# Kernel optimization log

Hardware: AMD Instinct MI355X
Metric: run time of the kernel (lower is better)

Reference implementation:

```python
import jax, jax.numpy as jnp
import numpy as np

EPS = 1e-5
N_HEADS = 8

def _layernorm(h, g, b):
    mu = jnp.mean(h, axis=-1, keepdims=True)
    var = jnp.mean((h - mu) ** 2, axis=-1, keepdims=True)
    return g * (h - mu) * jax.lax.rsqrt(var + EPS) + b

def _mlp_ln(x, W1, b1, W2, b2, g, beta):
    # Linear -> SiLU -> Linear -> LayerNorm (torch nn.Sequential processor)
    h = jax.nn.silu(x @ W1.T + b1)
    h = h @ W2.T + b2
    return _layernorm(h, g, beta)

def setup_inputs() -> dict:
    key = jax.random.key(0)
    ks = jax.random.split(key, 16)
    B, S, D = 4, 2048, 1024
    M, P, C = 128, 256, 512
    def lin(k, o, i):
        return (jax.random.normal(k, (o, i), jnp.float32) / np.sqrt(i)).astype(jnp.float32)
    inp = {}
    inp['x'] = jax.random.normal(ks[0], (B, S, D), jnp.float32)
    inp['scale_types'] = jax.random.randint(ks[1], (B, S), 0, 3)
    for name, dim, k1, k2 in [('mol', M, 2, 3), ('path', P, 4, 5), ('cell', C, 6, 7)]:
        inp[name + '_W1'] = lin(ks[k1], dim, D)
        inp[name + '_b1'] = jnp.zeros((dim,), jnp.float32)
        inp[name + '_W2'] = lin(ks[k2], dim, dim)
        inp[name + '_b2'] = jnp.zeros((dim,), jnp.float32)
        inp[name + '_g'] = jnp.ones((dim,), jnp.float32)
        inp[name + '_beta'] = jnp.zeros((dim,), jnp.float32)
    inp['int_W1'] = lin(ks[8], D, M + P + C)
    inp['int_b1'] = jnp.zeros((D,), jnp.float32)
    inp['int_W2'] = lin(ks[9], D, D)
    inp['int_b2'] = jnp.zeros((D,), jnp.float32)
    inp['int_g'] = jnp.ones((D,), jnp.float32)
    inp['int_beta'] = jnp.zeros((D,), jnp.float32)
    inp['attn_Wqkv'] = lin(ks[10], 3 * D, D)
    inp['attn_bqkv'] = jnp.zeros((3 * D,), jnp.float32)
    inp['attn_Wo'] = lin(ks[11], D, D)
    inp['attn_bo'] = jnp.zeros((D,), jnp.float32)
    inp['scale_w'] = jnp.ones((3,), jnp.float32) / 3.0
    return inp

def reference(x, scale_types,
              mol_W1, mol_b1, mol_W2, mol_b2, mol_g, mol_beta,
              path_W1, path_b1, path_W2, path_b2, path_g, path_beta,
              cell_W1, cell_b1, cell_W2, cell_b2, cell_g, cell_beta,
              int_W1, int_b1, int_W2, int_b2, int_g, int_beta,
              attn_Wqkv, attn_bqkv, attn_Wo, attn_bo, scale_w):
    B, S, D = x.shape
    # per-token routing: each token goes through exactly one expert; the
    # other two scale outputs are zeros (mask instead of Python loop).
    mol = _mlp_ln(x, mol_W1, mol_b1, mol_W2, mol_b2, mol_g, mol_beta) * (scale_types == 0)[..., None]
    path = _mlp_ln(x, path_W1, path_b1, path_W2, path_b2, path_g, path_beta) * (scale_types == 1)[..., None]
    cell = _mlp_ln(x, cell_W1, cell_b1, cell_W2, cell_b2, cell_g, cell_beta) * (scale_types == 2)[..., None]
    cat = jnp.concatenate([mol, path, cell], axis=-1)  # [B,S,M+P+C]
    integrated = _layernorm(jax.nn.silu(cat @ int_W1.T + int_b1) @ int_W2.T + int_b2, int_g, int_beta)
    # torch nn.MultiheadAttention (batch_first, self-attention)
    Dh = D // N_HEADS
    qkv = integrated @ attn_Wqkv.T + attn_bqkv  # [B,S,3D]
    q, k, v = jnp.split(qkv, 3, axis=-1)
    q = q.reshape(B, S, N_HEADS, Dh)
    k = k.reshape(B, S, N_HEADS, Dh)
    v = v.reshape(B, S, N_HEADS, Dh)
    scores = jnp.einsum('bqhd,bkhd->bhqk', q, k) / np.sqrt(Dh).astype(np.float32)
    attn = jax.nn.softmax(scores, axis=-1)
    o = jnp.einsum('bhqk,bkhd->bqhd', attn, v).reshape(B, S, D)
    attended = o @ attn_Wo.T + attn_bo
    w = jax.nn.softmax(scale_w, axis=0)
    final = integrated + w[0] * attended
    return (final, mol, path, cell)
```

## Files before the change

### kernel.cpp

```cpp
#include <hip/hip_runtime.h>
#include <cstdint>
#include <cstddef>

typedef unsigned short u16;
typedef unsigned int u32;
typedef short bf16x8 __attribute__((ext_vector_type(8)));
typedef float f32x4 __attribute__((ext_vector_type(4)));

__device__ __forceinline__ float bf2f(u16 u){
  union { u32 i; float f; } c; c.i = ((u32)u) << 16; return c.f;
}
__device__ __forceinline__ u16 f2bf(float f){
  union { float f; u32 i; } c; c.f = f;
  u32 r = c.i + 0x7FFFu + ((c.i >> 16) & 1u);
  return (u16)(r >> 16);
}
__device__ __forceinline__ void gload_lds16(const void* g, void* l){
  __builtin_amdgcn_global_load_lds(
      (const __attribute__((address_space(1))) u32*)g,
      (__attribute__((address_space(3))) u32*)l, 16, 0, 0);
}

struct ConvArgs {
  const float* src[11];
  u16* dst[11];
  u32 base[12];
};
__global__ __launch_bounds__(256)
void f32_to_bf16_multi(ConvArgs a){
  u32 i = blockIdx.x * 256 + threadIdx.x;
  if (i >= a.base[11]) return;
  int j = 0;
  #pragma unroll
  for (int k = 1; k < 11; ++k) j += (i >= a.base[k]);
  u32 li = i - a.base[j];
  const float4* s = (const float4*)a.src[j] + (size_t)li * 2;
  float4 va = s[0], vb = s[1];
  u16 o[8] = {f2bf(va.x),f2bf(va.y),f2bf(va.z),f2bf(va.w),
              f2bf(vb.x),f2bf(vb.y),f2bf(vb.z),f2bf(vb.w)};
  *(uint4*)(a.dst[j] + (size_t)li * 8) = *(const uint4*)o;
}

__global__ __launch_bounds__(256)
void concat3_f32(const float* __restrict__ a, const float* __restrict__ b,
                 const float* __restrict__ c, float* __restrict__ d){
  int i = blockIdx.x * 256 + threadIdx.x;
  if (i < 128) d[i] = a[i];
  else if (i < 384) d[i] = b[i - 128];
  else if (i < 896) d[i] = c[i - 384];
}

template<int EPI>
__device__ __forceinline__ void gemm_body(
    const u16* __restrict__ A, const u16* __restrict__ W,
    const float* __restrict__ bias, void* __restrict__ Cv,
    int N, int K, int lda, int ldc,
    const u16* __restrict__ I, const float* __restrict__ sw,
    int bx, int by)
{
  __shared__ __align__(16) u16 As[128*64];
  __shared__ __align__(16) u16 Bs[128*64];
  const int tid  = threadIdx.x;
  const int lane = tid & 63;
  const int wave = tid >> 6;
  const int wr = wave >> 1, wc = wave & 1;
  const int m0 = by * 128, n0 = bx * 128;

  f32x4 acc[4][4];
  #pragma unroll
  for (int r=0;r<4;++r)
    #pragma unroll
    for (int c=0;c<4;++c)
      #pragma unroll
      for (int e=0;e<4;++e) acc[r][c][e] = 0.f;

  int srow[4], soff[4];
  #pragma unroll
  for (int j=0;j<4;++j){
    int rr = (wave*4 + j)*8 + (lane>>3);
    srow[j] = rr;
    soff[j] = ((lane & 7) ^ (rr & 7)) * 8;
  }

  for (int k0 = 0; k0 < K; k0 += 64){
    #pragma unroll
    for (int j=0;j<4;++j){
      gload_lds16(A + (size_t)(m0 + srow[j])*lda + k0 + soff[j], As + (wave*4+j)*512);
      gload_lds16(W + (size_t)(n0 + srow[j])*K   + k0 + soff[j], Bs + (wave*4+j)*512);
    }
    __syncthreads();
    #pragma unroll
    for (int ks=0; ks<2; ++ks){
      bf16x8 af[4], bfr[4];
      #pragma unroll
      for (int r=0;r<4;++r){
        int row = wr*64 + r*16 + (lane&15);
        int cs  = (ks*4 + (lane>>4)) ^ (row & 7);
        af[r] = *(const bf16x8*)(As + row*64 + cs*8);
      }
      #pragma unroll
      for (int c=0;c<4;++c){
        int row = wc*64 + c*16 + (lane&15);
        int cs  = (ks*4 + (lane>>4)) ^ (row & 7);
        bfr[c] = *(const bf16x8*)(Bs + row*64 + cs*8);
      }
      #pragma unroll
      for (int r=0;r<4;++r)
        #pragma unroll
        for (int c=0;c<4;++c)
          acc[r][c] = __builtin_amdgcn_mfma_f32_16x16x32_bf16(af[r], bfr[c], acc[r][c], 0,0,0);
    }
    __syncthreads();
  }

  float w0 = 0.f;
  if (EPI == 2){
    float s0 = sw[0], s1 = sw[1], s2 = sw[2];
    float mx = fmaxf(s0, fmaxf(s1, s2));
    float e0 = __expf(s0-mx), e1 = __expf(s1-mx), e2 = __expf(s2-mx);
    w0 = e0 / (e0 + e1 + e2);
  }
  u16*   C16 = (u16*)Cv;
  float* C32 = (float*)Cv;
  #pragma unroll
  for (int c=0;c<4;++c){
    int col = n0 + wc*64 + c*16 + (lane&15);
    float bv = bias[col];
    #pragma unroll
    for (int r=0;r<4;++r){
      int rbase = m0 + wr*64 + r*16 + (lane>>4)*4;
      #pragma unroll
      for (int e=0;e<4;++e){
        int row = rbase + e;
        float v = acc[r][c][e] + bv;
        if (EPI == 1) v = v / (1.f + __expf(-v));
        if (EPI == 2){
          v = bf2f(I[(size_t)row*ldc + col]) + w0 * v;
          C32[(size_t)row*ldc + col] = v;
        } else {
          C16[(size_t)row*ldc + col] = f2bf(v);
        }
      }
    }
  }
}

template<int EPI>
__global__ __launch_bounds__(256, 2)
void gemm_bt(const u16* __restrict__ A, const u16* __restrict__ W,
             const float* __restrict__ bias, void* __restrict__ Cv,
             int N, int K, int lda, int ldc,
             const u16* __restrict__ I, const float* __restrict__ sw)
{
  gemm_body<EPI>(A, W, bias, Cv, N, K, lda, ldc, I, sw, blockIdx.x, blockIdx.y);
}

__global__ __launch_bounds__(256, 2)
void gemm_w2group(const u16* __restrict__ S1, u16* __restrict__ S2,
                  const u16* __restrict__ w0, const u16* __restrict__ w1,
                  const u16* __restrict__ w2, const float* __restrict__ b0,
                  const float* __restrict__ b1, const float* __restrict__ b2)
{
  int bx = blockIdx.x;
  if (bx < 64){
    gemm_body<0>(S1, w0, b0, S2, 128, 128, 896, 896, nullptr, nullptr, 0, bx);
  } else if (bx < 192){
    int l = bx - 64;
    gemm_body<0>(S1+128, w1, b1, S2+128, 256, 256, 896, 896, nullptr, nullptr, l>>6, l&63);
  } else {
    int l = bx - 192;
    gemm_body<0>(S1+384, w2, b2, S2+384, 512, 512, 896, 896, nullptr, nullptr, l>>6, l&63);
  }
}

template<int D>
__device__ __forceinline__ void ln_body_masked(
    u16* __restrict__ H, int ldh, const float* __restrict__ g,
    const float* __restrict__ beta, const int* __restrict__ st,
    int eid, float* __restrict__ outp)
{
  const int tid = threadIdx.x, lane = tid & 63, wave = tid >> 6;
  const int token = blockIdx.x * 4 + wave;
  constexpr int VPT = D / 64;
  float v[VPT];
  u16* row = H + (size_t)token * ldh + lane * VPT;
  #pragma unroll
  for (int i=0;i<VPT/2;++i){
    u32 u = ((const u32*)row)[i];
    v[2*i]   = bf2f((u16)(u & 0xFFFFu));
    v[2*i+1] = bf2f((u16)(u >> 16));
  }
  float s = 0.f;
  #pragma unroll
  for (int i=0;i<VPT;++i) s += v[i];
  #pragma unroll
  for (int off=1; off<64; off<<=1) s += __shfl_xor(s, off);
  float mu = s * (1.f / D);
  float q = 0.f;
  #pragma unroll
  for (int i=0;i<VPT;++i){ float d = v[i] - mu; q += d * d; }
  #pragma unroll
  for (int off=1; off<64; off<<=1) q += __shfl_xor(q, off);
  float rs = rsqrtf(q * (1.f / D) + 1e-5f);
  float msk = (st[token] == eid) ? 1.f : 0.f;
  #pragma unroll
  for (int i=0;i<VPT;++i){
    float gg = g[lane*VPT + i];
    float bb = beta[lane*VPT + i];
    float val = (gg * (v[i] - mu) * rs + bb) * msk;
    outp[(size_t)token * D + lane * VPT + i] = val;
    row[i] = f2bf(val);
  }
}

__global__ __launch_bounds__(256, 4)
void ln_expert(u16* __restrict__ S2,
               const float* __restrict__ g0, const float* __restrict__ be0,
               const float* __restrict__ g1, const float* __restrict__ be1,
               const float* __restrict__ g2, const float* __restrict__ be2,
               const int* __restrict__ st,
               float* __restrict__ o0, float* __restrict__ o1,
               float* __restrict__ o2)
{
  if (blockIdx.y == 0)      ln_body_masked<128>(S2,     896, g0, be0, st, 0, o0);
  else if (blockIdx.y == 1) ln_body_masked<256>(S2+128, 896, g1, be1, st, 1, o1);
  else                      ln_body_masked<512>(S2+384, 896, g2, be2, st, 2, o2);
}

__global__ __launch_bounds__(256, 4)
void ln_int(const u16* __restrict__ H, const float* __restrict__ g,
            const float* __restrict__ beta, u16* __restrict__ outp)
{
  const int tid = threadIdx.x, lane = tid & 63, wave = tid >> 6;
  const int token = blockIdx.x * 4 + wave;
  constexpr int D = 1024, VPT = 16;
  float v[VPT];
  const u16* row = H + (size_t)token * D + lane * VPT;
  #pragma unroll
  for (int i=0;i<VPT/2;++i){
    u32 u = ((const u32*)row)[i];
    v[2*i]   = bf2f((u16)(u & 0xFFFFu));
    v[2*i+1] = bf2f((u16)(u >> 16));
  }
  float s = 0.f;
  #pragma unroll
  for (int i=0;i<VPT;++i) s += v[i];
  #pragma unroll
  for (int off=1; off<64; off<<=1) s += __shfl_xor(s, off);
  float mu = s * (1.f / D);
  float q = 0.f;
  #pragma unroll
  for (int i=0;i<VPT;++i){ float d = v[i] - mu; q += d * d; }
  #pragma unroll
  for (int off=1; off<64; off<<=1) q += __shfl_xor(q, off);
  float rs = rsqrtf(q * (1.f / D) + 1e-5f);
  #pragma unroll
  for (int i=0;i<VPT;++i){
    float val = g[lane*VPT + i] * (v[i] - mu) * rs + beta[lane*VPT + i];
    outp[(size_t)token * D + lane * VPT + i] = f2bf(val);
  }
}

__global__ __launch_bounds__(256)
void transpose_v(const u16* __restrict__ qkv, u16* __restrict__ vt)
{
  __shared__ __align__(16) u16 T[64*72];
  const int tid = threadIdx.x;
  const int tt = blockIdx.x;
  const int dt = blockIdx.y;
  const int bh = blockIdx.z;
  const int b = bh >> 3, h = bh & 7;
  #pragma unroll
  for (int i=0;i<2;++i){
    int idx = tid + 256*i;
    int r = idx >> 3, c8 = idx & 7;
    const uint4* src = (const uint4*)(qkv + (size_t)(b*2048 + tt*64 + r)*3072
                                      + 2048 + h*128 + dt*64 + c8*8);
    *(uint4*)(T + r*72 + ((c8 ^ (r>>3)) & 7)*8) = *src;
  }
  __syncthreads();
  #pragma unroll
  for (int i=0;i<2;++i){
    int idx = tid + 256*i;
    int dr = idx >> 3, tc = idx & 7;
    u16 tmp[8];
    #pragma unroll
    for (int j=0;j<8;++j){
      int kap = tc*8 + j;
      int hp = kap >> 5, r2 = kap & 31;
      int srow = hp*32 + ((r2 & 1) ? 16 + (r2 >> 1) : (r2 >> 1));
      tmp[j] = T[srow*72 + (((dr>>3) ^ (srow>>3)) & 7)*8 + (dr & 7)];
    }
    *(uint4*)(vt + ((size_t)bh*128 + dt*64 + dr)*2048 + tt*64 + tc*8) = *(const uint4*)tmp;
  }
}

__global__ __launch_bounds__(256, 4)
void flash_attn(const u16* __restrict__ qkv, const u16* __restrict__ vt,
                u16* __restrict__ o)
{
  __shared__ __align__(16) u16 Ks[8192];
  __shared__ __align__(16) u16 Vs[8192];
  __shared__ __align__(16) u16 Ps[4*1024];
  const int tid = threadIdx.x, lane = tid & 63, wave = tid >> 6;
  const int b = blockIdx.z, h = blockIdx.y, q0 = blockIdx.x * 64;
  const float cl2   = 0.12751791892f;
  const float DEFER = 90.50966799187809f;

  bf16x8 qreg[4];
  {
    const u16* qrow = qkv + (size_t)(b*2048 + q0 + wave*16 + (lane&15))*3072
                      + h*128 + (lane>>4)*8;
    #pragma unroll
    for (int kk=0;kk<4;++kk) qreg[kk] = *(const bf16x8*)(qrow + kk*32);
  }
  asm volatile("s_waitcnt vmcnt(0)" ::: "memory");

  const u16* ksrc[4]; const u16* vsrc[4]; int cdst[4];
  #pragma unroll
  for (int i=0;i<4;++i){
    int cidx = (wave*4 + i)*64 + lane;
    int krow = cidx >> 4, kcs = cidx & 15;
    int kcsrc = (kcs & 8) | ((kcs & 7) ^ (krow & 7));
    ksrc[i] = qkv + (size_t)(b*2048 + krow)*3072 + h*128 + 1024 + kcsrc*8;
    int vd = cidx >> 3, vcs = cidx & 7;
    vsrc[i] = vt + ((size_t)(b*8 + h)*128 + vd)*2048 + (vcs ^ (vd & 7))*8;
    cdst[i] = cidx * 8;
  }

  int koff[16];
  #pragma unroll
  for (int kk=0;kk<4;++kk)
    #pragma unroll
    for (int cb=0;cb<4;++cb){
      int row  = (lane&15) + 16*cb;
      int c    = kk*4 + (lane>>4);
      int slot = (c & 8) | ((c & 7) ^ (row & 7));
      koff[kk*4+cb] = (row*128 + slot*8) * 2;
    }
  int voff[16];
  #pragma unroll
  for (int kk=0;kk<2;++kk)
    #pragma unroll
    for (int f=0;f<8;++f){
      int d = f*16 + (lane&15);
      int c = kk*4 + (lane>>4);
      voff[kk*8+f] = (d*64 + (c ^ (d & 7))*8) * 2;
    }
  int pwoff[8];
  #pragma unroll
  for (int e=0;e<4;++e){
    int prow = (lane>>4)*4 + e;
    int j01 = lane & 15;
    int j23 = 16 + (lane & 15);
    pwoff[e*2]   = (prow*32 + (((((j01>>2) ^ (prow&7)) & 7)<<2) | (j01&3))) * 4;
    pwoff[e*2+1] = (prow*32 + (((((j23>>2) ^ (prow&7)) & 7)<<2) | (j23&3))) * 4;
  }
  int proff[2];
  #pragma unroll
  for (int kk=0;kk<2;++kk){
    int prow = lane & 15;
    int pc   = kk*4 + (lane>>4);
    proff[kk] = (prow*64 + ((pc ^ (prow & 7)) & 7)*8) * 2;
  }

  auto stageK = [&](int kt){
    #pragma unroll
    for (int i=0;i<4;++i) gload_lds16(ksrc[i] + (size_t)kt*196608, Ks + cdst[i]);
  };
  auto stageV = [&](int kt){
    #pragma unroll
    for (int i=0;i<4;++i) gload_lds16(vsrc[i] + kt*64, Vs + cdst[i]);
  };

  f32x4 oacc[8];
  #pragma unroll
  for (int f=0;f<8;++f)
    #pragma unroll
    for (int e=0;e<4;++e) oacc[f][e] = 0.f;
  float m_run[4] = {-3e38f,-3e38f,-3e38f,-3e38f};
  float l_run[4] = {0.f,0.f,0.f,0.f};
  const char* KsB = (const char*)Ks;
  const char* VsB = (const char*)Vs;
  char* PsWB = (char*)(Ps + wave*1024);

  stageK(0);
  stageV(0);
  asm volatile("s_waitcnt vmcnt(4)" ::: "memory");
  __builtin_amdgcn_s_barrier();
  __builtin_amdgcn_sched_barrier(0);

  for (int kt=0; kt<32; ++kt){
    f32x4 s[4];
    #pragma unroll
    for (int cb=0;cb<4;++cb)
      #pragma unroll
      for (int e=0;e<4;++e) s[cb][e] = 0.f;
    __builtin_amdgcn_s_setprio(1);
    #pragma unroll
    for (int kk=0;kk<4;++kk){
      #pragma unroll
      for (int cb=0;cb<4;++cb){
        bf16x8 bk = *(const bf16x8*)(KsB + koff[kk*4+cb]);
        s[cb] = __builtin_amdgcn_mfma_f32_16x16x32_bf16(qreg[kk], bk, s[cb], 0,0,0);
      }
    }
    __builtin_amdgcn_s_setprio(0);
    asm volatile("s_waitcnt lgkmcnt(0)" ::: "memory");
    __builtin_amdgcn_sched_barrier(0);
    __builtin_amdgcn_s_barrier();
    __builtin_amdgcn_sched_barrier(0);
    stageK((kt+1)&31);

    #pragma unroll
    for (int e=0;e<4;++e){
      float t0 = s[0][e], t1 = s[1][e], t2 = s[2][e], t3 = s[3][e];
      float lmx = fmaxf(fmaxf(t0,t1), fmaxf(t2,t3));
      if (__any(lmx > m_run[e] + DEFER)){
        float mx = lmx;
        #pragma unroll
        for (int off=1; off<16; off<<=1) mx = fmaxf(mx, __shfl_xor(mx, off));
        float mnew = fmaxf(m_run[e], mx);
        float a = exp2f((m_run[e] - mnew) * cl2);
        m_run[e] = mnew;
        l_run[e] *= a;
        #pragma unroll
        for (int f=0;f<8;++f) oacc[f][e] *= a;
      }
      float ms = m_run[e];
      float p0 = exp2f((t0 - ms)*cl2), p1 = exp2f((t1 - ms)*cl2);
      float p2 = exp2f((t2 - ms)*cl2), p3 = exp2f((t3 - ms)*cl2);
      l_run[e] += (p0 + p1) + (p2 + p3);
      u32 c01, c23;
      asm("v_cvt_pk_bf16_f32 %0, %1, %2" : "=v"(c01) : "v"(p0), "v"(p1));
      asm("v_cvt_pk_bf16_f32 %0, %1, %2" : "=v"(c23) : "v"(p2), "v"(p3));
      *(u32*)(PsWB + pwoff[e*2])   = c01;
      *(u32*)(PsWB + pwoff[e*2+1]) = c23;
    }

    asm volatile("s_waitcnt vmcnt(4)" ::: "memory");
    __builtin_amdgcn_sched_barrier(0);
    __builtin_amdgcn_s_barrier();
    __builtin_amdgcn_sched_barrier(0);

    __builtin_amdgcn_s_setprio(1);
    #pragma unroll
    for (int kk=0;kk<2;++kk){
      bf16x8 pa = *(const bf16x8*)(PsWB + proff[kk]);
      #pragma unroll
      for (int f=0;f<8;++f){
        bf16x8 vb = *(const bf16x8*)(VsB + voff[kk*8+f]);
        oacc[f] = __builtin_amdgcn_mfma_f32_16x16x32_bf16(pa, vb, oacc[f], 0,0,0);
      }
    }
    __builtin_amdgcn_s_setprio(0);
    asm volatile("s_waitcnt lgkmcnt(0) vmcnt(0)" ::: "memory");
    __builtin_amdgcn_sched_barrier(0);
    __builtin_amdgcn_s_barrier();
    __builtin_amdgcn_sched_barrier(0);
    if (kt + 1 < 32) stageV(kt+1);
  }

  #pragma unroll
  for (int e=0;e<4;++e){
    float l = l_run[e];
    #pragma unroll
    for (int off=1; off<16; off<<=1) l += __shfl_xor(l, off);
    l_run[e] = 1.f / l;
  }
  #pragma unroll
  for (int f=0;f<8;++f)
    #pragma unroll
    for (int e=0;e<4;++e){
      int row = q0 + wave*16 + (lane>>4)*4 + e;
      int col = h*128 + f*16 + (lane&15);
      o[(size_t)(b*2048 + row)*1024 + col] = f2bf(oacc[f][e] * l_run[e]);
    }
}

extern "C" void kernel_launch(void* const* d_in, const int* in_sizes, int n_in,
                              void* d_out, int out_size, void* d_ws, size_t ws_size,
                              hipStream_t stream)
{
  const float* x         = (const float*)d_in[0];
  const int*   stypes    = (const int*)d_in[1];
  const float* mol_W1    = (const float*)d_in[2];
  const float* mol_b1    = (const float*)d_in[3];
  const float* mol_W2    = (const float*)d_in[4];
  const float* mol_b2    = (const float*)d_in[5];
  const float* mol_g     = (const float*)d_in[6];
  const float* mol_beta  = (const float*)d_in[7];
  const float* path_W1   = (const float*)d_in[8];
  const float* path_b1   = (const float*)d_in[9];
  const float* path_W2   = (const float*)d_in[10];
  const float* path_b2   = (const float*)d_in[11];
  const float* path_g    = (const float*)d_in[12];
  const float* path_beta = (const float*)d_in[13];
  const float* cell_W1   = (const float*)d_in[14];
  const float* cell_b1   = (const float*)d_in[15];
  const float* cell_W2   = (const float*)d_in[16];
  const float* cell_b2   = (const float*)d_in[17];
  const float* cell_g    = (const float*)d_in[18];
  const float* cell_beta = (const float*)d_in[19];
  const float* int_W1    = (const float*)d_in[20];
  const float* int_b1    = (const float*)d_in[21];
  const float* int_W2    = (const float*)d_in[22];
  const float* int_b2    = (const float*)d_in[23];
  const float* int_g     = (const float*)d_in[24];
  const float* int_beta  = (const float*)d_in[25];
  const float* attn_Wqkv = (const float*)d_in[26];
  const float* attn_bqkv = (const float*)d_in[27];
  const float* attn_Wo   = (const float*)d_in[28];
  const float* attn_bo   = (const float*)d_in[29];
  const float* scale_w   = (const float*)d_in[30];

  float* out_final = (float*)d_out;
  float* out_mol   = out_final + 8388608;
  float* out_path  = out_mol   + 1048576;
  float* out_cell  = out_path  + 2097152;

  u16* ws    = (u16*)d_ws;
  u16* qkv   = ws;
  u16* integ = qkv   + 25165824;
  u16* S1    = integ + 8388608;
  u16* S2    = S1    + 8388608;
  u16* wb    = S2    + 8388608;
  u16* xb    = qkv;

  u16* w1f    = wb;
  u16* molW2b = w1f    + 917504;
  u16* pathW2b= molW2b + 16384;
  u16* cellW2b= pathW2b+ 65536;
  u16* intW1b = cellW2b+ 262144;
  u16* intW2b = intW1b + 917504;
  u16* qkvWb  = intW2b + 1048576;
  u16* woWb   = qkvWb  + 3145728;
  float* fbias= (float*)(woWb + 1048576);

  dim3 blk(256);

  ConvArgs ca;
  const float* srcs[11] = {x, mol_W1, path_W1, cell_W1, mol_W2, path_W2,
                           cell_W2, int_W1, int_W2, attn_Wqkv, attn_Wo};
  u16* dsts[11] = {xb, w1f, w1f + 131072, w1f + 393216, molW2b, pathW2b,
                   cellW2b, intW1b, intW2b, qkvWb, woWb};
  u32 n8s[11] = {1048576, 16384, 32768, 65536, 2048, 8192,
                 32768, 114688, 131072, 393216, 131072};
  u32 acc8 = 0;
  for (int i=0;i<11;++i){ ca.src[i]=srcs[i]; ca.dst[i]=dsts[i]; ca.base[i]=acc8; acc8+=n8s[i]; }
  ca.base[11] = acc8;
  f32_to_bf16_multi<<<(acc8 + 255)/256, blk, 0, stream>>>(ca);
  concat3_f32<<<4, blk, 0, stream>>>(mol_b1, path_b1, cell_b1, fbias);

  gemm_bt<1><<<dim3(7,64), blk, 0, stream>>>(xb, w1f, fbias, S1, 896, 1024, 1024, 896, nullptr, nullptr);
  gemm_w2group<<<448, blk, 0, stream>>>(S1, S2, molW2b, pathW2b, cellW2b,
                                        mol_b2, path_b2, cell_b2);
  ln_expert<<<dim3(2048,3), blk, 0, stream>>>(S2, mol_g, mol_beta, path_g,
                                              path_beta, cell_g, cell_beta,
                                              stypes, out_mol, out_path, out_cell);

  gemm_bt<1><<<dim3(8,64), blk, 0, stream>>>(S2, intW1b, int_b1, S1, 1024, 896,  896,  1024, nullptr, nullptr);
  gemm_bt<0><<<dim3(8,64), blk, 0, stream>>>(S1, intW2b, int_b2, S2, 1024, 1024, 1024, 1024, nullptr, nullptr);
  ln_int<<<2048, blk, 0, stream>>>(S2, int_g, int_beta, integ);

  gemm_bt<0><<<dim3(24,64), blk, 0, stream>>>(integ, qkvWb, attn_bqkv, qkv, 3072, 1024, 1024, 3072, nullptr, nullptr);
  transpose_v<<<dim3(32,2,32), blk, 0, stream>>>(qkv, S2);
  flash_attn<<<dim3(32,8,4), blk, 0, stream>>>(qkv, S2, S1);

  gemm_bt<2><<<dim3(8,64), blk, 0, stream>>>(S1, woWb, attn_bo, out_final, 1024, 1024, 1024, 1024, integ, scale_w);
}
```

Measured before the change: 332.2 us.

## Fuse V transpose into QKV GEMM via swapped-operand V^T tile epilogue

The QKV projection now runs as one launch. The Q/K blocks use the normal GEMM. The V part is computed directly as Wv·integ^T, with an epilogue that writes the permuted transposed layout flash attention expects. This removes the separate transpose_v kernel and its extra read and write of V. The cost is a scattered 2-byte store pattern in the new epilogue. Separately, flash attention's K/V staging now advances pointers incrementally instead of recomputing offsets. After the last iteration the K prefetch no longer wraps to tile 0 and reads past the current batch's K range.

```diff
diff --git a/kernel.cpp b/kernel.cpp
--- a/kernel.cpp
+++ b/kernel.cpp
@@ -125,18 +125,29 @@
   #pragma unroll
   for (int c=0;c<4;++c){
     int col = n0 + wc*64 + c*16 + (lane&15);
-    float bv = bias[col];
+    float bv = 0.f;
+    size_t vtb = 0;
+    if (EPI == 3){
+      int tl = (col & 2047) >> 6, pos = col & 63;
+      int p2 = pos & 31, hp = pos >> 5;
+      int kap = hp*32 + (p2 < 16 ? 2*p2 : 2*(p2-16)+1);
+      vtb = (size_t)(col >> 11) * 2097152 + (size_t)(tl*64 + kap);
+    } else {
+      bv = bias[col];
+    }
     #pragma unroll
     for (int r=0;r<4;++r){
       int rbase = m0 + wr*64 + r*16 + (lane>>4)*4;
       #pragma unroll
       for (int e=0;e<4;++e){
         int row = rbase + e;
-        float v = acc[r][c][e] + bv;
+        float v = acc[r][c][e] + (EPI==3 ? bias[row] : bv);
         if (EPI == 1) v = v / (1.f + __expf(-v));
         if (EPI == 2){
           v = bf2f(I[(size_t)row*ldc + col]) + w0 * v;
           C32[(size_t)row*ldc + col] = v;
+        } else if (EPI == 3){
+          C16[vtb + (size_t)row*2048] = f2bf(v);
         } else {
           C16[(size_t)row*ldc + col] = f2bf(v);
         }
@@ -173,6 +184,22 @@
   }
 }
 
+__global__ __launch_bounds__(256, 2)
+void gemm_qkv_vt(const u16* __restrict__ integ, const u16* __restrict__ Wqkv,
+                 const float* __restrict__ bqkv, u16* __restrict__ qkv,
+                 u16* __restrict__ vt)
+{
+  int bx = blockIdx.x;
+  if (bx < 1024){
+    gemm_body<0>(integ, Wqkv, bqkv, qkv, 2048, 1024, 1024, 3072,
+                 nullptr, nullptr, bx & 15, bx >> 4);
+  } else {
+    int l = bx - 1024;
+    gemm_body<3>(Wqkv + (size_t)2048*1024, integ, bqkv + 2048, vt, 8192, 1024,
+                 1024, 2048, nullptr, nullptr, l & 63, l >> 6);
+  }
+}
+
 template<int D>
 __device__ __forceinline__ void ln_body_masked(
     u16* __restrict__ H, int ldh, const float* __restrict__ g,
@@ -261,40 +288,6 @@
   }
 }
 
-__global__ __launch_bounds__(256)
-void transpose_v(const u16* __restrict__ qkv, u16* __restrict__ vt)
-{
-  __shared__ __align__(16) u16 T[64*72];
-  const int tid = threadIdx.x;
-  const int tt = blockIdx.x;
-  const int dt = blockIdx.y;
-  const int bh = blockIdx.z;
-  const int b = bh >> 3, h = bh & 7;
-  #pragma unroll
-  for (int i=0;i<2;++i){
-    int idx = tid + 256*i;
-    int r = idx >> 3, c8 = idx & 7;
-    const uint4* src = (const uint4*)(qkv + (size_t)(b*2048 + tt*64 + r)*3072
-                                      + 2048 + h*128 + dt*64 + c8*8);
-    *(uint4*)(T + r*72 + ((c8 ^ (r>>3)) & 7)*8) = *src;
-  }
-  __syncthreads();
-  #pragma unroll
-  for (int i=0;i<2;++i){
-    int idx = tid + 256*i;
-    int dr = idx >> 3, tc = idx & 7;
-    u16 tmp[8];
-    #pragma unroll
-    for (int j=0;j<8;++j){
-      int kap = tc*8 + j;
-      int hp = kap >> 5, r2 = kap & 31;
-      int srow = hp*32 + ((r2 & 1) ? 16 + (r2 >> 1) : (r2 >> 1));
-      tmp[j] = T[srow*72 + (((dr>>3) ^ (srow>>3)) & 7)*8 + (dr & 7)];
-    }
-    *(uint4*)(vt + ((size_t)bh*128 + dt*64 + dr)*2048 + tt*64 + tc*8) = *(const uint4*)tmp;
-  }
-}
-
 __global__ __launch_bounds__(256, 4)
 void flash_attn(const u16* __restrict__ qkv, const u16* __restrict__ vt,
                 u16* __restrict__ o)
@@ -364,13 +357,13 @@
     proff[kk] = (prow*64 + ((pc ^ (prow & 7)) & 7)*8) * 2;
   }
 
-  auto stageK = [&](int kt){
-    #pragma unroll
-    for (int i=0;i<4;++i) gload_lds16(ksrc[i] + (size_t)kt*196608, Ks + cdst[i]);
+  auto stageK = [&](){
+    #pragma unroll
+    for (int i=0;i<4;++i){ gload_lds16(ksrc[i], Ks + cdst[i]); ksrc[i] += 196608; }
   };
-  auto stageV = [&](int kt){
-    #pragma unroll
-    for (int i=0;i<4;++i) gload_lds16(vsrc[i] + kt*64, Vs + cdst[i]);
+  auto stageV = [&](){
+    #pragma unroll
+    for (int i=0;i<4;++i){ gload_lds16(vsrc[i], Vs + cdst[i]); vsrc[i] += 64; }
   };
 
   f32x4 oacc[8];
@@ -384,8 +377,8 @@
   const char* VsB = (const char*)Vs;
   char* PsWB = (char*)(Ps + wave*1024);
 
-  stageK(0);
-  stageV(0);
+  stageK();
+  stageV();
   asm volatile("s_waitcnt vmcnt(4)" ::: "memory");
   __builtin_amdgcn_s_barrier();
   __builtin_amdgcn_sched_barrier(0);
@@ -410,7 +403,7 @@
     __builtin_amdgcn_sched_barrier(0);
     __builtin_amdgcn_s_barrier();
     __builtin_amdgcn_sched_barrier(0);
-    stageK((kt+1)&31);
+    stageK();
 
     #pragma unroll
     for (int e=0;e<4;++e){
@@ -458,7 +451,7 @@
     __builtin_amdgcn_sched_barrier(0);
     __builtin_amdgcn_s_barrier();
     __builtin_amdgcn_sched_barrier(0);
-    if (kt + 1 < 32) stageV(kt+1);
+    if (kt + 1 < 32) stageV();
   }
 
   #pragma unroll
@@ -563,8 +556,7 @@
   gemm_bt<0><<<dim3(8,64), blk, 0, stream>>>(S1, intW2b, int_b2, S2, 1024, 1024, 1024, 1024, nullptr, nullptr);
   ln_int<<<2048, blk, 0, stream>>>(S2, int_g, int_beta, integ);
 
-  gemm_bt<0><<<dim3(24,64), blk, 0, stream>>>(integ, qkvWb, attn_bqkv, qkv, 3072, 1024, 1024, 3072, nullptr, nullptr);
-  transpose_v<<<dim3(32,2,32), blk, 0, stream>>>(qkv, S2);
+  gemm_qkv_vt<<<1536, blk, 0, stream>>>(integ, qkvWb, attn_bqkv, qkv, S2);
   flash_attn<<<dim3(32,8,4), blk, 0, stream>>>(qkv, S2, S1);
 
   gemm_bt<2><<<dim3(8,64), blk, 0, stream>>>(S1, woWb, attn_bo, out_final, 1024, 1024, 1024, 1024, integ, scale_w);
```

After: 329.6 us. About the same (-0.8%).
